# Optimization experiments

Hardware: AMD Instinct MI355X
Metric: run time of the kernel (lower is better)

Reference implementation:

```python
import jax, jax.numpy as jnp
import numpy as np

B, S, D_ENC, D_DEC, UNITS = 32, 2048, 1024, 1024, 1024


def setup_inputs() -> dict:
    key = jax.random.key(0)
    k1, k2, k3, k4 = jax.random.split(key, 4)
    h_encoder = jax.random.normal(k1, (B, S, D_ENC), dtype=jnp.float32)
    h_decoder_prev = jax.random.normal(k2, (B, D_DEC), dtype=jnp.float32)
    # Dense1: (D_ENC + D_DEC) -> UNITS, tanh; Dense2: UNITS -> 1, relu
    W1 = jax.random.normal(k3, (D_ENC + D_DEC, UNITS), dtype=jnp.float32) * 0.02
    b1 = jnp.zeros((UNITS,), dtype=jnp.float32)
    W2 = jax.random.normal(k4, (UNITS, 1), dtype=jnp.float32) * 0.02
    b2 = jnp.zeros((1,), dtype=jnp.float32)
    return {"h_encoder": h_encoder, "h_decoder_prev": h_decoder_prev,
            "W1": W1, "b1": b1, "W2": W2, "b2": b2}


def reference(h_encoder, h_decoder_prev, W1, b1, W2, b2):
    # Equivalent to concat([h_encoder, repeat(h_decoder)], -1) @ W1 without
    # materializing the repeated/concatenated tensor: split W1 by input block.
    d_enc = h_encoder.shape[-1]
    W1_enc, W1_dec = W1[:d_enc], W1[d_enc:]
    dec_proj = h_decoder_prev @ W1_dec  # [B, UNITS]
    energies1 = jnp.tanh(jnp.einsum('bse,eu->bsu', h_encoder, W1_enc)
                         + dec_proj[:, None, :] + b1)  # [B, S, UNITS]
    energies2 = jax.nn.relu(jnp.einsum('bsu,uo->bso', energies1, W2) + b2)  # [B, S, 1]
    attention_weights = jax.nn.softmax(energies2, axis=1)  # softmax over seq axis
    # repeat along last dim + multiply + reduce_sum == broadcast-weighted sum
    context_vector = jnp.sum(attention_weights * h_encoder, axis=1)  # [B, D_ENC]
    return (context_vector, attention_weights)
```

## Files before the change

### kernel.cpp

```cpp
#include <hip/hip_runtime.h>
#include <cstdint>
#include <cstddef>

#define BB 32
#define SS 2048
#define DD 1024
#define MM (BB * SS)

typedef __bf16 bf16_t;
typedef __bf16 bf16x4 __attribute__((ext_vector_type(4)));
typedef __bf16 bf16x8 __attribute__((ext_vector_type(8)));
typedef float  f32x4  __attribute__((ext_vector_type(4)));

typedef __attribute__((address_space(1))) unsigned int gu32;
typedef __attribute__((address_space(3))) unsigned int lu32;

__device__ __forceinline__ void async_copy16(const void* g, void* l) {
  __builtin_amdgcn_global_load_lds((gu32*)g, (lu32*)l, 16, 0, 0);
}

__global__ __launch_bounds__(256) void conv_w1t_kernel(
    const float* __restrict__ W1, bf16_t* __restrict__ W1T) {
  __shared__ float tile[64][65];
  const int bk = (blockIdx.x & 15) * 64;
  const int bn = (blockIdx.x >> 4) * 64;
  const int tx = threadIdx.x & 63;
  const int ty = threadIdx.x >> 6;
#pragma unroll
  for (int i = 0; i < 16; ++i) {
    const int kr = i * 4 + ty;
    tile[kr][tx] = W1[(size_t)(bk + kr) * 1024 + bn + tx];
  }
  __syncthreads();
#pragma unroll
  for (int i = 0; i < 16; ++i) {
    const int nr = i * 4 + ty;
    W1T[(size_t)(bn + nr) * 1024 + bk + tx] = (bf16_t)tile[tx][nr];
  }
}

__global__ __launch_bounds__(256) void dec_proj_kernel(
    const float* __restrict__ hDec, const float* __restrict__ W1,
    const float* __restrict__ b1, float* __restrict__ dp) {
  __shared__ float sred[256];
  const int bidx = blockIdx.x;
  const int b  = bidx >> 3;
  const int uc = bidx & 7;
  const int t  = threadIdx.x;
  const int u  = uc * 128 + (t & 127);
  const int kh = t >> 7;
  const float* wd = W1 + (size_t)1024 * 1024 + u;
  const float* hd = hDec + b * 1024 + kh * 512;
  float acc = 0.f;
#pragma unroll 4
  for (int k = 0; k < 512; ++k)
    acc += hd[k] * wd[(size_t)(kh * 512 + k) * 1024];
  sred[t] = acc;
  __syncthreads();
  if (t < 128) dp[b * 1024 + u] = sred[t] + sred[t + 128] + b1[u];
}

__global__ __launch_bounds__(256, 2) void fused_gemm_v3(
    const float* __restrict__ hEnc, const bf16_t* __restrict__ W1T,
    const float* __restrict__ dp, const float* __restrict__ W2,
    float* __restrict__ e2p) {
  __shared__ bf16_t sA[128 * 64];
  __shared__ bf16_t sB[2][128 * 64];

  const int tid  = threadIdx.x;
  const int lane = tid & 63;
  const int wv   = tid >> 6;
  const int wm   = wv >> 1;
  const int wn   = wv & 1;

  const int bid   = blockIdx.x;
  const int mtile = ((bid >> 6) << 3) | (bid & 7);
  const int nblk  = (bid >> 3) & 7;
  const int m0    = mtile * 128;
  const int n0    = nblk * 128;
  const int b     = m0 >> 11;

  const int col = lane & 15;
  const int q   = lane >> 4;
  const int sw  = q ^ ((col >> 1) & 3);

  f32x4 acc[4][4];
#pragma unroll
  for (int mi = 0; mi < 4; ++mi)
#pragma unroll
    for (int ni = 0; ni < 4; ++ni)
      acc[mi][ni] = (f32x4){0.f, 0.f, 0.f, 0.f};

  char* sAc = (char*)sA;
  char* sBc = (char*)&sB[0][0];

  const int lrow = lane >> 2;
  const int lc   = (lane & 3) ^ ((lane >> 3) & 3);
  const int s0   = wv * 2, s1 = wv * 2 + 1;
  const bf16_t* bG0 = W1T + (size_t)(n0 + s0 * 16 + lrow) * 1024 + lc * 8;
  const bf16_t* bG1 = W1T + (size_t)(n0 + s1 * 16 + lrow) * 1024 + lc * 8;

  const int r0  = tid >> 3;
  const int oct = tid & 7;
  const float* aG = hEnc + (size_t)(m0 + r0) * 1024 + oct * 8;
  const unsigned wOff = (unsigned)(((oct >> 2) * 8192) + r0 * 64 +
                                   (((oct & 3) ^ ((r0 >> 1) & 3)) << 4));

  const unsigned a_rd = (unsigned)((wm * 64 + col) * 64 + sw * 16);
  const unsigned b_rd = (unsigned)((wn * 64 + col) * 64 + sw * 16);

  async_copy16(bG0,      sBc + s0 * 1024);
  async_copy16(bG1,      sBc + s1 * 1024);
  async_copy16(bG0 + 32, sBc + 8192 + s0 * 1024);
  async_copy16(bG1 + 32, sBc + 8192 + s1 * 1024);
  float4 ar[4][2];
#pragma unroll
  for (int i = 0; i < 4; ++i) {
    ar[i][0] = *(const float4*)(aG + (size_t)i * 32 * 1024);
    ar[i][1] = *(const float4*)(aG + (size_t)i * 32 * 1024 + 4);
  }

  int c = 0;
#pragma unroll 1
  for (int t = 0; t < 16; ++t) {
#pragma unroll
    for (int i = 0; i < 4; ++i) {
      bf16x8 a8;
      a8[0] = (bf16_t)ar[i][0].x; a8[1] = (bf16_t)ar[i][0].y;
      a8[2] = (bf16_t)ar[i][0].z; a8[3] = (bf16_t)ar[i][0].w;
      a8[4] = (bf16_t)ar[i][1].x; a8[5] = (bf16_t)ar[i][1].y;
      a8[6] = (bf16_t)ar[i][1].z; a8[7] = (bf16_t)ar[i][1].w;
      *(bf16x8*)(sAc + wOff + i * 2048) = a8;
    }
    __syncthreads();

    if (t < 15) {
      const int kn = t * 64 + 64;
      char* nb = sBc + (c ^ 1) * 16384;
      async_copy16(bG0 + kn,      nb + s0 * 1024);
      async_copy16(bG1 + kn,      nb + s1 * 1024);
      async_copy16(bG0 + kn + 32, nb + 8192 + s0 * 1024);
      async_copy16(bG1 + kn + 32, nb + 8192 + s1 * 1024);
#pragma unroll
      for (int i = 0; i < 4; ++i) {
        ar[i][0] = *(const float4*)(aG + kn + (size_t)i * 32 * 1024);
        ar[i][1] = *(const float4*)(aG + kn + (size_t)i * 32 * 1024 + 4);
      }
    }

    const char* sBr = sBc + c * 16384;
#pragma unroll
    for (int pl = 0; pl < 2; ++pl) {
      bf16x8 af[4], bf[4];
#pragma unroll
      for (int mi = 0; mi < 4; ++mi)
        af[mi] = *(const bf16x8*)(sAc + pl * 8192 + a_rd + mi * 1024);
#pragma unroll
      for (int ni = 0; ni < 4; ++ni)
        bf[ni] = *(const bf16x8*)(sBr + pl * 8192 + b_rd + ni * 1024);
#pragma unroll
      for (int mi = 0; mi < 4; ++mi)
#pragma unroll
        for (int ni = 0; ni < 4; ++ni)
          acc[mi][ni] = __builtin_amdgcn_mfma_f32_16x16x32_bf16(af[mi], bf[ni], acc[mi][ni], 0, 0, 0);
    }
    __builtin_amdgcn_s_barrier();
    __builtin_amdgcn_sched_barrier(0);
    c ^= 1;
  }

  float rs[4][4];
#pragma unroll
  for (int mi = 0; mi < 4; ++mi)
#pragma unroll
    for (int r = 0; r < 4; ++r) rs[mi][r] = 0.f;

  const float* dpb = dp + b * 1024 + n0 + wn * 64 + col;
  const float* w2b = W2 + n0 + wn * 64 + col;
#pragma unroll
  for (int ni = 0; ni < 4; ++ni) {
    const float dpn = dpb[ni * 16];
    const float w2n = w2b[ni * 16];
#pragma unroll
    for (int mi = 0; mi < 4; ++mi)
#pragma unroll
      for (int r = 0; r < 4; ++r) {
        const float x = acc[mi][ni][r] + dpn;
        const float e = __expf(2.f * x);
        const float th = 1.f - 2.f / (e + 1.f);
        rs[mi][r] += th * w2n;
      }
  }
#pragma unroll
  for (int off = 1; off < 16; off <<= 1)
#pragma unroll
    for (int mi = 0; mi < 4; ++mi)
#pragma unroll
      for (int r = 0; r < 4; ++r)
        rs[mi][r] += __shfl_xor(rs[mi][r], off, 64);
  if (col == 0) {
    float* dst = e2p + (size_t)(nblk * 2 + wn) * MM + m0 + wm * 64 + q * 4;
#pragma unroll
    for (int mi = 0; mi < 4; ++mi) {
      f32x4 o4 = {rs[mi][0], rs[mi][1], rs[mi][2], rs[mi][3]};
      *(f32x4*)(dst + mi * 16) = o4;
    }
  }
}

__global__ __launch_bounds__(256) void softmax_v2(
    const float* __restrict__ e2p, const float* __restrict__ b2,
    float* __restrict__ attn) {
  const int b = blockIdx.x;
  const int t = threadIdx.x;
  __shared__ float sred[4];
  const float b2v = b2[0];
  float v[8];
  float lmax = 0.f;
#pragma unroll
  for (int i = 0; i < 8; ++i) {
    const float* p = e2p + b * 2048 + i * 256 + t;
    float s = 0.f;
#pragma unroll
    for (int ps = 0; ps < 16; ++ps) s += p[(size_t)ps * MM];
    v[i] = fmaxf(s + b2v, 0.f);
    lmax = fmaxf(lmax, v[i]);
  }
#pragma unroll
  for (int off = 1; off < 64; off <<= 1) lmax = fmaxf(lmax, __shfl_xor(lmax, off, 64));
  const int wv = t >> 6;
  const int lane = t & 63;
  if (lane == 0) sred[wv] = lmax;
  __syncthreads();
  const float bmax = fmaxf(fmaxf(sred[0], sred[1]), fmaxf(sred[2], sred[3]));
  __syncthreads();
  float ev[8];
  float lsum = 0.f;
#pragma unroll
  for (int i = 0; i < 8; ++i) { ev[i] = __expf(v[i] - bmax); lsum += ev[i]; }
#pragma unroll
  for (int off = 1; off < 64; off <<= 1) lsum += __shfl_xor(lsum, off, 64);
  if (lane == 0) sred[wv] = lsum;
  __syncthreads();
  const float inv = 1.f / (sred[0] + sred[1] + sred[2] + sred[3]);
#pragma unroll
  for (int i = 0; i < 8; ++i) attn[b * 2048 + i * 256 + t] = ev[i] * inv;
}

__global__ __launch_bounds__(256) void context_v3(
    const float* __restrict__ hEnc, const float* __restrict__ attn,
    float* __restrict__ ctxp) {
  const int b = blockIdx.x >> 3;
  const int cks = blockIdx.x & 7;
  const int t = threadIdx.x;
  __shared__ float w[256];
  w[t] = attn[b * 2048 + cks * 256 + t];
  __syncthreads();
  float ax = 0.f, ay = 0.f, az = 0.f, aw = 0.f;
  const float* base = hEnc + ((size_t)b * 2048 + cks * 256) * 1024 + t * 4;
#pragma unroll 8
  for (int s = 0; s < 256; ++s) {
    const float4 h4 = *(const float4*)(base + (size_t)s * 1024);
    const float ws = w[s];
    ax += ws * h4.x; ay += ws * h4.y; az += ws * h4.z; aw += ws * h4.w;
  }
  f32x4 o4 = {ax, ay, az, aw};
  *(f32x4*)(ctxp + (size_t)cks * 32768 + b * 1024 + t * 4) = o4;
}

__global__ __launch_bounds__(256) void ctx_reduce8(
    const float* __restrict__ ctxp, float* __restrict__ ctx) {
  const int idx = blockIdx.x * 256 + threadIdx.x;
  f32x4 s = {0.f, 0.f, 0.f, 0.f};
#pragma unroll
  for (int p = 0; p < 8; ++p)
    s += *(const f32x4*)(ctxp + (size_t)p * 32768 + (size_t)idx * 4);
  *(f32x4*)(ctx + (size_t)idx * 4) = s;
}

extern "C" void kernel_launch(void* const* d_in, const int* in_sizes, int n_in,
                              void* d_out, int out_size, void* d_ws, size_t ws_size,
                              hipStream_t stream) {
  const float* hEnc = (const float*)d_in[0];
  const float* hDec = (const float*)d_in[1];
  const float* W1   = (const float*)d_in[2];
  const float* b1   = (const float*)d_in[3];
  const float* W2   = (const float*)d_in[4];
  const float* b2   = (const float*)d_in[5];
  float* out = (float*)d_out;

  char* ws = (char*)d_ws;
  bf16_t* W1T  = (bf16_t*)ws;
  float*  dp   = (float*)(ws + 2u * 1024 * 1024);
  float*  e2p  = (float*)(ws + 2u * 1024 * 1024 + 128u * 1024);
  float*  ctxp = (float*)(ws + 6u * 1024 * 1024 + 128u * 1024);

  conv_w1t_kernel<<<256, 256, 0, stream>>>(W1, W1T);
  dec_proj_kernel<<<256, 256, 0, stream>>>(hDec, W1, b1, dp);
  fused_gemm_v3<<<4096, 256, 0, stream>>>(hEnc, W1T, dp, W2, e2p);
  softmax_v2<<<32, 256, 0, stream>>>(e2p, b2, out + 32768);
  context_v3<<<256, 256, 0, stream>>>(hEnc, out + 32768, ctxp);
  ctx_reduce8<<<32, 256, 0, stream>>>(ctxp, out);
}
```

Baseline: 614.1 us.

## Reschedule GEMM A/B staging and raise occupancy to three blocks per CU

```diff
diff --git a/kernel.cpp b/kernel.cpp
--- a/kernel.cpp
+++ b/kernel.cpp
@@ -60,7 +60,7 @@
   if (t < 128) dp[b * 1024 + u] = sred[t] + sred[t + 128] + b1[u];
 }
 
-__global__ __launch_bounds__(256, 2) void fused_gemm_v3(
+__global__ __launch_bounds__(256, 3) void fused_gemm_v4(
     const float* __restrict__ hEnc, const bf16_t* __restrict__ W1T,
     const float* __restrict__ dp, const float* __restrict__ W2,
     float* __restrict__ e2p) {
@@ -100,53 +100,55 @@
   const bf16_t* bG0 = W1T + (size_t)(n0 + s0 * 16 + lrow) * 1024 + lc * 8;
   const bf16_t* bG1 = W1T + (size_t)(n0 + s1 * 16 + lrow) * 1024 + lc * 8;
 
-  const int r0  = tid >> 3;
-  const int oct = tid & 7;
-  const float* aG = hEnc + (size_t)(m0 + r0) * 1024 + oct * 8;
-  const unsigned wOff = (unsigned)(((oct >> 2) * 8192) + r0 * 64 +
-                                   (((oct & 3) ^ ((r0 >> 1) & 3)) << 4));
+  const int frow = tid >> 3;
+  const int fc   = tid & 7;
+  const float* aG = hEnc + (size_t)(m0 + frow) * 1024 + fc * 4;
+  const unsigned wBase = (unsigned)(frow * 64 +
+      (((fc >> 1) ^ ((frow >> 1) & 3)) << 4) + (fc & 1) * 8);
 
   const unsigned a_rd = (unsigned)((wm * 64 + col) * 64 + sw * 16);
   const unsigned b_rd = (unsigned)((wn * 64 + col) * 64 + sw * 16);
 
-  async_copy16(bG0,      sBc + s0 * 1024);
-  async_copy16(bG1,      sBc + s1 * 1024);
-  async_copy16(bG0 + 32, sBc + 8192 + s0 * 1024);
-  async_copy16(bG1 + 32, sBc + 8192 + s1 * 1024);
   float4 ar[4][2];
-#pragma unroll
-  for (int i = 0; i < 4; ++i) {
-    ar[i][0] = *(const float4*)(aG + (size_t)i * 32 * 1024);
-    ar[i][1] = *(const float4*)(aG + (size_t)i * 32 * 1024 + 4);
-  }
+
+#define STAGE_B(kk, bufc) do { char* nb = sBc + (bufc) * 16384;     \
+    async_copy16(bG0 + (kk),      nb + s0 * 1024);                  \
+    async_copy16(bG1 + (kk),      nb + s1 * 1024);                  \
+    async_copy16(bG0 + (kk) + 32, nb + 8192 + s0 * 1024);           \
+    async_copy16(bG1 + (kk) + 32, nb + 8192 + s1 * 1024); } while (0)
+
+#define LOAD_A(kk) do {                                             \
+    _Pragma("unroll")                                               \
+    for (int i = 0; i < 4; ++i) {                                   \
+      ar[i][0] = *(const float4*)(aG + (kk) + (size_t)i * 32768);   \
+      ar[i][1] = *(const float4*)(aG + (kk) + 32 + (size_t)i * 32768); \
+    } } while (0)
+
+  STAGE_B(0, 0);
+  LOAD_A(0);
 
   int c = 0;
 #pragma unroll 1
   for (int t = 0; t < 16; ++t) {
+    if (t < 15) STAGE_B(t * 64 + 64, c ^ 1);
+
 #pragma unroll
     for (int i = 0; i < 4; ++i) {
-      bf16x8 a8;
-      a8[0] = (bf16_t)ar[i][0].x; a8[1] = (bf16_t)ar[i][0].y;
-      a8[2] = (bf16_t)ar[i][0].z; a8[3] = (bf16_t)ar[i][0].w;
-      a8[4] = (bf16_t)ar[i][1].x; a8[5] = (bf16_t)ar[i][1].y;
-      a8[6] = (bf16_t)ar[i][1].z; a8[7] = (bf16_t)ar[i][1].w;
-      *(bf16x8*)(sAc + wOff + i * 2048) = a8;
-    }
-    __syncthreads();
-
-    if (t < 15) {
-      const int kn = t * 64 + 64;
-      char* nb = sBc + (c ^ 1) * 16384;
-      async_copy16(bG0 + kn,      nb + s0 * 1024);
-      async_copy16(bG1 + kn,      nb + s1 * 1024);
-      async_copy16(bG0 + kn + 32, nb + 8192 + s0 * 1024);
-      async_copy16(bG1 + kn + 32, nb + 8192 + s1 * 1024);
-#pragma unroll
-      for (int i = 0; i < 4; ++i) {
-        ar[i][0] = *(const float4*)(aG + kn + (size_t)i * 32 * 1024);
-        ar[i][1] = *(const float4*)(aG + kn + (size_t)i * 32 * 1024 + 4);
+#pragma unroll
+      for (int pl = 0; pl < 2; ++pl) {
+        const float4 v = ar[i][pl];
+        bf16x4 a4;
+        a4[0] = (bf16_t)v.x; a4[1] = (bf16_t)v.y;
+        a4[2] = (bf16_t)v.z; a4[3] = (bf16_t)v.w;
+        *(bf16x4*)(sAc + pl * 8192 + wBase + i * 2048) = a4;
       }
     }
+    asm volatile("s_waitcnt lgkmcnt(0)" ::: "memory");
+    __builtin_amdgcn_sched_barrier(0);
+    __builtin_amdgcn_s_barrier();
+    __builtin_amdgcn_sched_barrier(0);
+
+    if (t < 15) LOAD_A(t * 64 + 64);
 
     const char* sBr = sBc + c * 16384;
 #pragma unroll
@@ -168,6 +170,8 @@
     __builtin_amdgcn_sched_barrier(0);
     c ^= 1;
   }
+#undef STAGE_B
+#undef LOAD_A
 
   float rs[4][4];
 #pragma unroll
@@ -297,7 +301,7 @@
 
   conv_w1t_kernel<<<256, 256, 0, stream>>>(W1, W1T);
   dec_proj_kernel<<<256, 256, 0, stream>>>(hDec, W1, b1, dp);
-  fused_gemm_v3<<<4096, 256, 0, stream>>>(hEnc, W1T, dp, W2, e2p);
+  fused_gemm_v4<<<4096, 256, 0, stream>>>(hEnc, W1T, dp, W2, e2p);
   softmax_v2<<<32, 256, 0, stream>>>(e2p, b2, out + 32768);
   context_v3<<<256, 256, 0, stream>>>(hEnc, out + 32768, ctxp);
   ctx_reduce8<<<32, 256, 0, stream>>>(ctxp, out);
```

Measured after the change: 597.8 us. 2.7% less time.
